# Kernel tuning notes

Hardware: AMD Instinct MI355X
Metric: run time of the kernel (lower is better)

The kernel has to match this reference:

```python
import jax, jax.numpy as jnp
import numpy as np

# Model dims derived from layers=[1024,2048,2048,2048,2048]
B = 4096
SUM_EVEN = 4096  # 0 + 2048 + 2048
SUM_ODD = 4096   # 2048 + 2048
D1 = 2048        # layers[1]: width of Ux
BLK = 2048


def rho(x):
    return jax.nn.sigmoid(4.0 * (x - 0.5))


def make_mask():
    # Staircase block pattern from layer_slices():
    # (rows 0:2048, cols 0:2048), (rows 0:2048, cols 2048:4096), (rows 2048:4096, cols 2048:4096)
    m = np.zeros((SUM_EVEN, SUM_ODD), dtype=np.float32)
    m[0:BLK, 0:BLK] = 1.0
    m[0:BLK, BLK:2 * BLK] = 1.0
    m[BLK:2 * BLK, BLK:2 * BLK] = 1.0
    return jnp.asarray(m)


def setup_inputs() -> dict:
    key = jax.random.key(0)
    k1, k2, k3 = jax.random.split(key, 3)
    xavier_std = 0.02  # ~ sqrt(2/(2048+2048)) per block
    W_mask = make_mask()
    W_tensor = jax.random.normal(k1, (SUM_EVEN, SUM_ODD), jnp.float32) * xavier_std
    W_tensor = W_tensor * W_mask  # enforce staircase sparsity at init
    return {
        "Ux": jax.random.normal(k2, (B, D1), jnp.float32),
        "s": jax.random.normal(k3, (B, SUM_EVEN), jnp.float32),
        "W_tensor": W_tensor,
        "b_even": jnp.zeros((1, SUM_EVEN), jnp.float32),
        "b_odd": jnp.zeros((1, SUM_ODD), jnp.float32),
        "W_mask": W_mask,
    }


def reference(Ux, s, W_tensor, b_even, b_odd, W_mask):
    # s_new = rho(rho(s) @ W + b_odd [+ Ux on first D1 cols]) @ W.T + b_even
    W = W_tensor * W_mask  # masked staircase matrix
    s_odd = rho(s) @ W + b_odd                 # [B, SUM_ODD]
    s_odd = s_odd.at[:, :D1].add(Ux)           # x only feeds first hidden layer
    return rho(s_odd) @ W.T + b_even           # [B, SUM_EVEN]
```

## Files before the change

### kernel.cpp

```cpp
#include <hip/hip_runtime.h>
#include <hip/hip_bf16.h>


#define N_DIM 4096
#define D1_DIM 2048

typedef short short8 __attribute__((ext_vector_type(8)));
typedef float f32x4 __attribute__((ext_vector_type(4)));

__device__ __forceinline__ float rho_f(float x) {
    return 1.0f / (1.0f + __expf(2.0f - 4.0f * x));
}

__device__ __forceinline__ unsigned short f2bf(float x) {
    unsigned int u = __builtin_bit_cast(unsigned int, x);
    u += 0x7fffu + ((u >> 16) & 1u);
    return (unsigned short)(u >> 16);
}

__device__ __forceinline__ void gl_lds16(const unsigned short* g, void* l) {
    __builtin_amdgcn_global_load_lds(
        (const __attribute__((address_space(1))) void*)g,
        (__attribute__((address_space(3))) void*)l, 16, 0, 0);
}

__global__ __launch_bounds__(256) void prep_kernel(
    const float* __restrict__ s, const float* __restrict__ W,
    unsigned short* __restrict__ Rs, unsigned short* __restrict__ Wb,
    unsigned short* __restrict__ WTb) {
    __shared__ unsigned short t[32][33];
    const int id = blockIdx.x;
    if (id < 16384) {
        const int bx = id & 127, by = id >> 7;
        if (by * 32 >= D1_DIM && bx * 32 < D1_DIM) return;
        const int tx = threadIdx.x & 31, ty = threadIdx.x >> 5;
        const int x = bx * 32 + tx;
        #pragma unroll
        for (int r = 0; r < 4; r++) {
            const int y = by * 32 + ty + r * 8;
            const size_t idx = (size_t)y * N_DIM + x;
            const unsigned short b = f2bf(W[idx]);
            Wb[idx] = b;
            t[ty + r * 8][tx] = b;
        }
        __syncthreads();
        #pragma unroll
        for (int r = 0; r < 4; r++) {
            const int yy = ty + r * 8;
            WTb[(size_t)(bx * 32 + yy) * N_DIM + (by * 32 + tx)] = t[tx][yy];
        }
    } else {
        const int n8 = (N_DIM * N_DIM) / 8;
        const int stride = 2048 * 256;
        for (int i = (id - 16384) * 256 + threadIdx.x; i < n8; i += stride) {
            float4 a = ((const float4*)s)[2 * i];
            float4 b = ((const float4*)s)[2 * i + 1];
            unsigned int r0 = f2bf(rho_f(a.x)) | ((unsigned int)f2bf(rho_f(a.y)) << 16);
            unsigned int r1 = f2bf(rho_f(a.z)) | ((unsigned int)f2bf(rho_f(a.w)) << 16);
            unsigned int r2 = f2bf(rho_f(b.x)) | ((unsigned int)f2bf(rho_f(b.y)) << 16);
            unsigned int r3 = f2bf(rho_f(b.z)) | ((unsigned int)f2bf(rho_f(b.w)) << 16);
            uint4 o; o.x = r0; o.y = r1; o.z = r2; o.w = r3;
            ((uint4*)Rs)[i] = o;
        }
    }
}

template<int MODE>
__global__ __launch_bounds__(1024, 4) void gemm_kernel(
    const unsigned short* __restrict__ A,
    const unsigned short* __restrict__ Bt,
    void* __restrict__ Out,
    const float* __restrict__ Ux,
    const float* __restrict__ bias) {
    __shared__ __align__(16) char lds[163840];

    const int id = blockIdx.x;
    const int wg = ((id & 7) << 5) | (id >> 3);
    const int by = wg >> 4, bx = wg & 15;
    const int brow = by << 8, bcol = bx << 8;

    const int tid = threadIdx.x;
    const int w = tid >> 6;
    const int L = tid & 63;
    const int wr = w >> 2;
    const int wc = w & 3;
    const int fr = L & 15;
    const int fq = L >> 4;
    const int swz = fr & 7;

    int kbeg, kend;
    if (MODE == 1) { kbeg = 0; kend = (bcol < D1_DIM) ? D1_DIM : N_DIM; }
    else           { kbeg = (bcol < D1_DIM) ? 0 : D1_DIM; kend = N_DIM; }

    const int srl = w * 8 + (L >> 3);
    const int schunk8 = ((L & 7) ^ (L >> 3)) << 3;
    const int wbase = w * 1024;
#define STAGEF(mat, gb, kcol, base) do {                                       \
        const unsigned short* g0_ = (mat) +                                    \
            (size_t)((gb) + srl) * N_DIM + (kcol) + schunk8;                   \
        gl_lds16(g0_, lds + (base) + wbase);                                   \
        gl_lds16(g0_ + 128 * N_DIM, lds + (base) + 16384 + wbase);             \
    } while (0)

    short8 af[2][4], bf[4];
#define LDA_K(ab, ks) do {                                                     \
        _Pragma("unroll") for (int m_ = 0; m_ < 4; ++m_) {                     \
            const int R_ = wr * 64 + m_ * 16 + fr;                             \
            af[ks][m_] = *(const short8*)(lds + (ab) + R_ * 128 +              \
                ((((ks) * 4 + fq) ^ swz) << 4)); }                             \
    } while (0)
#define LDB_K(bb, ks) do {                                                     \
        _Pragma("unroll") for (int n_ = 0; n_ < 4; ++n_) {                     \
            const int R_ = wc * 64 + n_ * 16 + fr;                             \
            bf[n_] = *(const short8*)(lds + (bb) + R_ * 128 +                  \
                ((((ks) * 4 + fq) ^ swz) << 4)); }                             \
    } while (0)

    f32x4 acc[4][4];
    #pragma unroll
    for (int i = 0; i < 4; i++)
        #pragma unroll
        for (int j = 0; j < 4; j++)
            acc[i][j] = (f32x4){0.f, 0.f, 0.f, 0.f};

#define MFMA_K(ks) do {                                                        \
        __builtin_amdgcn_s_setprio(1);                                         \
        _Pragma("unroll") for (int m_ = 0; m_ < 4; ++m_)                       \
        _Pragma("unroll") for (int n_ = 0; n_ < 4; ++n_)                       \
            acc[m_][n_] = __builtin_amdgcn_mfma_f32_16x16x32_bf16(             \
                af[ks][m_], bf[n_], acc[m_][n_], 0, 0, 0);                     \
        __builtin_amdgcn_s_setprio(0);                                         \
    } while (0)

#define SBAR0() __builtin_amdgcn_sched_barrier(0)
#define LGKM(n) do { asm volatile("s_waitcnt lgkmcnt(" #n ")" ::: "memory");   \
                     SBAR0(); } while (0)
#define BAR() __builtin_amdgcn_s_barrier()

    const int nk = (kend - kbeg) >> 6;
    const int km = nk - 1;

    {
        const int k0 = kbeg;
        const int k1 = kbeg + ((1 & km) << 6);
        STAGEF(A, brow, k0, 0);       STAGEF(Bt, bcol, k0, 98304);
        STAGEF(A, brow, k1, 32768);   STAGEF(Bt, bcol, k1, 131072);
        asm volatile("s_waitcnt vmcnt(4)" ::: "memory");
        BAR();
    }

    int ai = 0, si = 2;
    for (int t = 0; t < nk; ++t) {
        const int aB = ai * 32768;
        const int sA = si * 32768;
        const int bB = 98304 + (t & 1) * 32768;
        const int ka = kbeg + (((t + 2) & km) << 6);

        STAGEF(A, brow, ka, sA);
        LDA_K(aB, 0); SBAR0();
        LDB_K(bB, 0); SBAR0();
        LDA_K(aB, 1); SBAR0();
        LGKM(4);
        MFMA_K(0);
        LDB_K(bB, 1); SBAR0();
        LGKM(0);
        MFMA_K(1);
        asm volatile("s_waitcnt vmcnt(2)" ::: "memory");
        BAR();
        STAGEF(Bt, bcol, ka, bB);
        ai++; if (ai == 3) ai = 0;
        si++; if (si == 3) si = 0;
    }
    asm volatile("s_waitcnt vmcnt(0)" ::: "memory");

    const bool hasUx = (MODE == 1) && (bcol < D1_DIM);
    #pragma unroll
    for (int m = 0; m < 4; m++) {
        const int row0 = brow + wr * 64 + m * 16 + fq * 4;
        #pragma unroll
        for (int n = 0; n < 4; n++) {
            const int col = bcol + wc * 64 + n * 16 + fr;
            const float bv = bias[col];
            #pragma unroll
            for (int r = 0; r < 4; r++) {
                const int row = row0 + r;
                float v = acc[m][n][r] + bv;
                if (MODE == 1) {
                    if (hasUx) v += Ux[(size_t)row * D1_DIM + col];
                    ((unsigned short*)Out)[(size_t)row * N_DIM + col] =
                        f2bf(rho_f(v));
                } else {
                    ((float*)Out)[(size_t)row * N_DIM + col] = v;
                }
            }
        }
    }
#undef STAGEF
#undef LDA_K
#undef LDB_K
#undef MFMA_K
#undef SBAR0
#undef LGKM
#undef BAR
}

extern "C" void kernel_launch(void* const* d_in, const int* in_sizes, int n_in,
                              void* d_out, int out_size, void* d_ws, size_t ws_size,
                              hipStream_t stream) {
    const float* Ux     = (const float*)d_in[0];
    const float* s      = (const float*)d_in[1];
    const float* W      = (const float*)d_in[2];
    const float* b_even = (const float*)d_in[3];
    const float* b_odd  = (const float*)d_in[4];

    char* ws = (char*)d_ws;
    const size_t SZ = (size_t)N_DIM * N_DIM * 2;
    unsigned short* Rs  = (unsigned short*)(ws);
    unsigned short* R2  = (unsigned short*)(ws + SZ);
    unsigned short* Wb  = (unsigned short*)(ws + 2 * SZ);
    unsigned short* WTb = (unsigned short*)(ws + 3 * SZ);

    prep_kernel<<<18432, 256, 0, stream>>>(s, W, Rs, Wb, WTb);
    gemm_kernel<1><<<256, 1024, 0, stream>>>(Rs, WTb, (void*)R2, Ux, b_odd);
    gemm_kernel<2><<<256, 1024, 0, stream>>>(R2, Wb, d_out, Ux, b_even);
}
```

Baseline: 240.1 us.

## Balance staircase GEMM work across blocks with split-K partials and flag sync

Each GEMM's block work is rebalanced so every workgroup does equal K work. Short-K tiles also compute a 1024-deep partial of a long-K tile into a scratch buffer, and the long-K tiles finish the remaining 3072 and add the partial after spinning on a per-tile release/acquire flag. This targets the load imbalance in the staircase mask, where half the tiles had twice the K loop of the others. The cost is extra fp32 partial traffic through the output buffer, a memset for the flags, and spin-wait dependencies that assume all 256 blocks are co-resident.

```diff
diff --git a/kernel.cpp b/kernel.cpp
--- a/kernel.cpp
+++ b/kernel.cpp
@@ -71,14 +71,13 @@
     const unsigned short* __restrict__ Bt,
     void* __restrict__ Out,
     const float* __restrict__ Ux,
-    const float* __restrict__ bias) {
+    const float* __restrict__ bias,
+    float* __restrict__ pbuf,
+    unsigned int* __restrict__ flags,
+    const int split) {
     __shared__ __align__(16) char lds[163840];
 
     const int id = blockIdx.x;
-    const int wg = ((id & 7) << 5) | (id >> 3);
-    const int by = wg >> 4, bx = wg & 15;
-    const int brow = by << 8, bcol = bx << 8;
-
     const int tid = threadIdx.x;
     const int w = tid >> 6;
     const int L = tid & 63;
@@ -88,21 +87,45 @@
     const int fq = L >> 4;
     const int swz = fr & 7;
 
-    int kbeg, kend;
-    if (MODE == 1) { kbeg = 0; kend = (bcol < D1_DIM) ? D1_DIM : N_DIM; }
-    else           { kbeg = (bcol < D1_DIM) ? 0 : D1_DIM; kend = N_DIM; }
-
     const int srl = w * 8 + (L >> 3);
     const int schunk8 = ((L & 7) ^ (L >> 3)) << 3;
     const int wbase = w * 1024;
-#define STAGEF(mat, gb, kcol, base) do {                                       \
-        const unsigned short* g0_ = (mat) +                                    \
-            (size_t)((gb) + srl) * N_DIM + (kcol) + schunk8;                   \
+
+    int brow, bcol;
+    int kbeg, nk;
+    int role = 0;
+    int bcolH = 0, pidx = 0;
+    if (split) {
+        const int i = id & 127;
+        const int by = i >> 3, bg = i & 7;
+        brow = by << 8;
+        pidx = i;
+        if (id < 128) {
+            role = 1;
+            if (MODE == 1) { bcol = bg << 8;          kbeg = 0;    bcolH = D1_DIM + (bg << 8); }
+            else           { bcol = D1_DIM + (bg << 8); kbeg = 2048; bcolH = bg << 8; }
+            nk = 32;
+        } else {
+            role = 2;
+            bcol = (MODE == 1) ? (D1_DIM + (bg << 8)) : (bg << 8);
+            kbeg = 1024; nk = 48;
+        }
+    } else {
+        const int wg = ((id & 7) << 5) | (id >> 3);
+        brow = (wg >> 4) << 8; bcol = (wg & 15) << 8;
+        if (MODE == 1) { kbeg = 0; nk = (bcol < D1_DIM) ? 32 : 64; }
+        else           { kbeg = (bcol < D1_DIM) ? 0 : D1_DIM; nk = (bcol < D1_DIM) ? 64 : 32;
+                         if (bcol < D1_DIM) kbeg = 0; else kbeg = D1_DIM; }
+    }
+
+    f32x4 acc[4][4];
+    short8 af[2][4], bf[4];
+
+#define STAGEF(rowbase, kcol, base) do {                                       \
+        const unsigned short* g0_ = (rowbase) + (kcol);                        \
         gl_lds16(g0_, lds + (base) + wbase);                                   \
         gl_lds16(g0_ + 128 * N_DIM, lds + (base) + 16384 + wbase);             \
     } while (0)
-
-    short8 af[2][4], bf[4];
 #define LDA_K(ab, ks) do {                                                     \
         _Pragma("unroll") for (int m_ = 0; m_ < 4; ++m_) {                     \
             const int R_ = wr * 64 + m_ * 16 + fr;                             \
@@ -115,14 +138,6 @@
             bf[n_] = *(const short8*)(lds + (bb) + R_ * 128 +                  \
                 ((((ks) * 4 + fq) ^ swz) << 4)); }                             \
     } while (0)
-
-    f32x4 acc[4][4];
-    #pragma unroll
-    for (int i = 0; i < 4; i++)
-        #pragma unroll
-        for (int j = 0; j < 4; j++)
-            acc[i][j] = (f32x4){0.f, 0.f, 0.f, 0.f};
-
 #define MFMA_K(ks) do {                                                        \
         __builtin_amdgcn_s_setprio(1);                                         \
         _Pragma("unroll") for (int m_ = 0; m_ < 4; ++m_)                       \
@@ -131,66 +146,123 @@
                 af[ks][m_], bf[n_], acc[m_][n_], 0, 0, 0);                     \
         __builtin_amdgcn_s_setprio(0);                                         \
     } while (0)
-
 #define SBAR0() __builtin_amdgcn_sched_barrier(0)
 #define LGKM(n) do { asm volatile("s_waitcnt lgkmcnt(" #n ")" ::: "memory");   \
                      SBAR0(); } while (0)
 #define BAR() __builtin_amdgcn_s_barrier()
 
-    const int nk = (kend - kbeg) >> 6;
-    const int km = nk - 1;
-
-    {
-        const int k0 = kbeg;
-        const int k1 = kbeg + ((1 & km) << 6);
-        STAGEF(A, brow, k0, 0);       STAGEF(Bt, bcol, k0, 98304);
-        STAGEF(A, brow, k1, 32768);   STAGEF(Bt, bcol, k1, 131072);
+    auto run_tiles = [&](int bc, int kb, int n) {
+        #pragma unroll
+        for (int i2 = 0; i2 < 4; i2++)
+            #pragma unroll
+            for (int j2 = 0; j2 < 4; j2++)
+                acc[i2][j2] = (f32x4){0.f, 0.f, 0.f, 0.f};
+        const unsigned short* Arow = A + (size_t)(brow + srl) * N_DIM + schunk8 + kb;
+        const unsigned short* Brow = Bt + (size_t)(bc + srl) * N_DIM + schunk8 + kb;
+        STAGEF(Arow, 0, 0);      STAGEF(Brow, 0, 98304);
+        STAGEF(Arow, 64, 32768); STAGEF(Brow, 64, 131072);
         asm volatile("s_waitcnt vmcnt(4)" ::: "memory");
         BAR();
-    }
-
-    int ai = 0, si = 2;
-    for (int t = 0; t < nk; ++t) {
-        const int aB = ai * 32768;
-        const int sA = si * 32768;
-        const int bB = 98304 + (t & 1) * 32768;
-        const int ka = kbeg + (((t + 2) & km) << 6);
-
-        STAGEF(A, brow, ka, sA);
-        LDA_K(aB, 0); SBAR0();
-        LDB_K(bB, 0); SBAR0();
-        LDA_K(aB, 1); SBAR0();
-        LGKM(4);
-        MFMA_K(0);
-        LDB_K(bB, 1); SBAR0();
-        LGKM(0);
-        MFMA_K(1);
-        asm volatile("s_waitcnt vmcnt(2)" ::: "memory");
+        int ai = 0, si = 2;
+        for (int t = 0; t < n; ++t) {
+            const int aB = ai * 32768;
+            const int sA = si * 32768;
+            const int bB = 98304 + (t & 1) * 32768;
+            const int t2 = (t + 2 < n) ? (t + 2) : (n - 1);
+            const int ka = t2 << 6;
+            STAGEF(Arow, ka, sA);
+            LDA_K(aB, 0); SBAR0();
+            LDB_K(bB, 0); SBAR0();
+            LDA_K(aB, 1); SBAR0();
+            LGKM(4);
+            MFMA_K(0);
+            LDB_K(bB, 1); SBAR0();
+            LGKM(0);
+            MFMA_K(1);
+            asm volatile("s_waitcnt vmcnt(2)" ::: "memory");
+            BAR();
+            STAGEF(Brow, ka, bB);
+            ai++; if (ai == 3) ai = 0;
+            si++; if (si == 3) si = 0;
+        }
+        asm volatile("s_waitcnt vmcnt(0)" ::: "memory");
         BAR();
-        STAGEF(Bt, bcol, ka, bB);
-        ai++; if (ai == 3) ai = 0;
-        si++; if (si == 3) si = 0;
-    }
-    asm volatile("s_waitcnt vmcnt(0)" ::: "memory");
-
-    const bool hasUx = (MODE == 1) && (bcol < D1_DIM);
-    #pragma unroll
-    for (int m = 0; m < 4; m++) {
-        const int row0 = brow + wr * 64 + m * 16 + fq * 4;
-        #pragma unroll
-        for (int n = 0; n < 4; n++) {
-            const int col = bcol + wc * 64 + n * 16 + fr;
-            const float bv = bias[col];
+    };
+
+    if (role == 1) {
+        run_tiles(bcol, kbeg, nk);
+        const bool hasUx = (MODE == 1);
+        #pragma unroll
+        for (int m = 0; m < 4; m++) {
+            const int row0 = brow + wr * 64 + m * 16 + fq * 4;
             #pragma unroll
-            for (int r = 0; r < 4; r++) {
-                const int row = row0 + r;
-                float v = acc[m][n][r] + bv;
-                if (MODE == 1) {
-                    if (hasUx) v += Ux[(size_t)row * D1_DIM + col];
-                    ((unsigned short*)Out)[(size_t)row * N_DIM + col] =
-                        f2bf(rho_f(v));
-                } else {
-                    ((float*)Out)[(size_t)row * N_DIM + col] = v;
+            for (int n = 0; n < 4; n++) {
+                const int col = bcol + wc * 64 + n * 16 + fr;
+                const float bv = bias[col];
+                #pragma unroll
+                for (int r = 0; r < 4; r++) {
+                    const int row = row0 + r;
+                    float v = acc[m][n][r] + bv;
+                    if (MODE == 1) {
+                        if (hasUx) v += Ux[(size_t)row * D1_DIM + col];
+                        ((unsigned short*)Out)[(size_t)row * N_DIM + col] = f2bf(rho_f(v));
+                    } else {
+                        ((float*)Out)[(size_t)row * N_DIM + col] = v;
+                    }
+                }
+            }
+        }
+        run_tiles(bcolH, 0, 16);
+        #pragma unroll
+        for (int m = 0; m < 4; m++) {
+            const int row0 = brow + wr * 64 + m * 16 + fq * 4;
+            #pragma unroll
+            for (int n = 0; n < 4; n++) {
+                const int col = bcolH + wc * 64 + n * 16 + fr;
+                #pragma unroll
+                for (int r = 0; r < 4; r++)
+                    pbuf[(size_t)(row0 + r) * N_DIM + col] = acc[m][n][r];
+            }
+        }
+        __syncthreads();
+        if (tid == 0) {
+            __threadfence();
+            __hip_atomic_store(&flags[pidx], 1u, __ATOMIC_RELEASE,
+                               __HIP_MEMORY_SCOPE_AGENT);
+        }
+    } else {
+        run_tiles(bcol, kbeg, nk);
+        if (role == 2) {
+            if (tid == 0) {
+                while (__hip_atomic_load(&flags[pidx], __ATOMIC_ACQUIRE,
+                                         __HIP_MEMORY_SCOPE_AGENT) == 0u)
+                    __builtin_amdgcn_s_sleep(2);
+                __threadfence();
+            }
+            __syncthreads();
+        }
+        const bool hasUx = (!split) && (MODE == 1) && (bcol < D1_DIM);
+        #pragma unroll
+        for (int m = 0; m < 4; m++) {
+            const int row0 = brow + wr * 64 + m * 16 + fq * 4;
+            #pragma unroll
+            for (int n = 0; n < 4; n++) {
+                const int col = bcol + wc * 64 + n * 16 + fr;
+                const float bv = bias[col];
+                #pragma unroll
+                for (int r = 0; r < 4; r++) {
+                    const int row = row0 + r;
+                    float v = acc[m][n][r] + bv;
+                    if (role == 2)
+                        v += __hip_atomic_load(&pbuf[(size_t)row * N_DIM + col],
+                                               __ATOMIC_RELAXED,
+                                               __HIP_MEMORY_SCOPE_AGENT);
+                    if (MODE == 1) {
+                        if (hasUx) v += Ux[(size_t)row * D1_DIM + col];
+                        ((unsigned short*)Out)[(size_t)row * N_DIM + col] = f2bf(rho_f(v));
+                    } else {
+                        ((float*)Out)[(size_t)row * N_DIM + col] = v;
+                    }
                 }
             }
         }
@@ -220,7 +292,15 @@
     unsigned short* Wb  = (unsigned short*)(ws + 2 * SZ);
     unsigned short* WTb = (unsigned short*)(ws + 3 * SZ);
 
+    const int split = (ws_size >= 4 * SZ + 4096) ? 1 : 0;
+    unsigned int* flags = (unsigned int*)(ws + 4 * SZ);
+    float* pbuf = (float*)d_out;
+    if (split)
+        hipMemsetAsync(flags, 0, 1024, stream);
+
     prep_kernel<<<18432, 256, 0, stream>>>(s, W, Rs, Wb, WTb);
-    gemm_kernel<1><<<256, 1024, 0, stream>>>(Rs, WTb, (void*)R2, Ux, b_odd);
-    gemm_kernel<2><<<256, 1024, 0, stream>>>(R2, Wb, d_out, Ux, b_even);
-}
+    gemm_kernel<1><<<256, 1024, 0, stream>>>(Rs, WTb, (void*)R2, Ux, b_odd,
+                                             pbuf, flags, split);
+    gemm_kernel<2><<<256, 1024, 0, stream>>>(R2, Wb, d_out, Ux, b_even,
+                                             pbuf, flags + 128, split);
+}
```

After: 611.8 us. 2.55x slower.
